# Optimization experiments

Hardware: AMD Instinct MI355X
Metric: run time of the kernel (lower is better)

## Reference

```python
import jax, jax.numpy as jnp
import numpy as np

B, N_LINKS, N_JOINTS, C_L, C_J = 4096, 33, 32, 64, 128

def setup_inputs() -> dict:
    key = jax.random.key(0)
    k1, k2, k3, k4 = jax.random.split(key, 4)
    link_feats = jax.random.normal(k1, (B, N_LINKS, C_L, 16), dtype=jnp.float32)
    joint_feats = jax.random.normal(k2, (B, N_JOINTS, C_J), dtype=jnp.float32)
    # Stacked per-joint Linear weights: [J, C_L*16, C_J], bias [J, C_J]
    fan_in = C_L * 16
    W = jax.random.normal(k3, (N_JOINTS, fan_in, C_J), dtype=jnp.float32) / np.sqrt(fan_in).astype(np.float32)
    b = jax.random.normal(k4, (N_JOINTS, C_J), dtype=jnp.float32) * 0.01
    child_idx = jnp.arange(1, N_JOINTS + 1, dtype=jnp.int64)  # child link of joint j is link j+1
    return {"link_feats": link_feats, "joint_feats": joint_feats, "W": W, "b": b, "child_idx": child_idx}

def reference(link_feats, joint_feats, W, b, child_idx):
    # Gather child-link features per joint: [B, J, C_L, 16] -> flatten to [B, J, C_L*16]
    Bsz = link_feats.shape[0]
    J = child_idx.shape[0]
    x = link_feats[:, child_idx].reshape(Bsz, J, -1)
    # Grouped GEMM over joints (replaces Python loop of tiny Linears), + bias + residual
    return jnp.einsum('bji,jio->bjo', x, W) + b[None, :, :] + joint_feats
```

## Files before the change

### kernel.cpp

```cpp
#include <hip/hip_runtime.h>

typedef __attribute__((ext_vector_type(8))) short bf16x8;
typedef __attribute__((ext_vector_type(4))) float f32x4;

#define NB    4096
#define NLINK 33
#define NJ    32
#define KTOT  1024
#define CJ    128
#define NSTEP 32

__device__ short g_Wf[NJ * KTOT * CJ];

static __device__ __forceinline__ short f2bf(float f) {
    unsigned u = __builtin_bit_cast(unsigned, f);
    unsigned r = u + 0x7FFFu + ((u >> 16) & 1u);
    return (short)(r >> 16);
}

__global__ __launch_bounds__(256) void conv_w(const float* __restrict__ W) {
    const int gid = blockIdx.x * 256 + threadIdx.x;
    const int q  = gid & 3;
    const int c  = (gid >> 2) & 127;
    const int kt = (gid >> 9) & 31;
    const int j  = gid >> 14;
    const float* src = W + ((size_t)j * KTOT + kt * 32 + q * 8) * CJ + c;
    bf16x8 v;
    #pragma unroll
    for (int e = 0; e < 8; ++e) v[e] = f2bf(src[(size_t)e * CJ]);
    reinterpret_cast<bf16x8*>(g_Wf)[gid] = v;
}

__global__ __launch_bounds__(256, 2) void joint_gemm(
    const float* __restrict__ link,
    const float* __restrict__ jf,
    const float* __restrict__ bias,
    const int*   __restrict__ child,
    float* __restrict__ out)
{
    const int tid  = threadIdx.x;
    const int lane = tid & 63;
    const int wave = tid >> 6;
    const int q    = lane >> 4;
    const int r    = lane & 15;

    const int bx = blockIdx.x;
    const int j  = bx & 31;
    const int mt = bx >> 5;
    const int row0 = mt * 128 + wave * 32;
    const int cidx = child[j];

    const float* a0 = link + ((size_t)(row0 + r) * NLINK + cidx) * KTOT + q * 8;
    const float* a1 = a0 + (size_t)16 * NLINK * KTOT;

    const bf16x8* wb = reinterpret_cast<const bf16x8*>(g_Wf);
    const size_t bb = ((size_t)j * 32 * 128 + r) * 4 + q;

    f32x4 acc[2][8] = {};

    float4 A0[4], A1[4];
    bf16x8 B0[8], B1[8];

    auto loadA = [&](float4* A, int t) {
        const float4* p0 = reinterpret_cast<const float4*>(a0 + t * 32);
        const float4* p1 = reinterpret_cast<const float4*>(a1 + t * 32);
        A[0] = p0[0]; A[1] = p0[1]; A[2] = p1[0]; A[3] = p1[1];
    };
    auto loadB = [&](bf16x8* Bv, int t) {
        const bf16x8* p = wb + bb + (size_t)t * 512;
        #pragma unroll
        for (int ni = 0; ni < 8; ++ni) Bv[ni] = p[ni * 64];
    };

    loadA(A0, 0); loadB(B0, 0);
    loadA(A1, 1); loadB(B1, 1);

    for (int t = 0; t < NSTEP; t += 2) {
        {
            bf16x8 af0, af1;
            const float* f = reinterpret_cast<const float*>(A0);
            #pragma unroll
            for (int e = 0; e < 8; ++e) { af0[e] = f2bf(f[e]); af1[e] = f2bf(f[8 + e]); }
            if (t + 2 < NSTEP) loadA(A0, t + 2);
            #pragma unroll
            for (int ni = 0; ni < 8; ++ni) {
                acc[0][ni] = __builtin_amdgcn_mfma_f32_16x16x32_bf16(af0, B0[ni], acc[0][ni], 0, 0, 0);
                acc[1][ni] = __builtin_amdgcn_mfma_f32_16x16x32_bf16(af1, B0[ni], acc[1][ni], 0, 0, 0);
            }
            if (t + 2 < NSTEP) loadB(B0, t + 2);
        }
        {
            bf16x8 af0, af1;
            const float* f = reinterpret_cast<const float*>(A1);
            #pragma unroll
            for (int e = 0; e < 8; ++e) { af0[e] = f2bf(f[e]); af1[e] = f2bf(f[8 + e]); }
            if (t + 3 < NSTEP) loadA(A1, t + 3);
            #pragma unroll
            for (int ni = 0; ni < 8; ++ni) {
                acc[0][ni] = __builtin_amdgcn_mfma_f32_16x16x32_bf16(af0, B1[ni], acc[0][ni], 0, 0, 0);
                acc[1][ni] = __builtin_amdgcn_mfma_f32_16x16x32_bf16(af1, B1[ni], acc[1][ni], 0, 0, 0);
            }
            if (t + 3 < NSTEP) loadB(B1, t + 3);
        }
    }

    float bv[8];
    #pragma unroll
    for (int ni = 0; ni < 8; ++ni) bv[ni] = bias[j * CJ + ni * 16 + r];

    #pragma unroll
    for (int mi = 0; mi < 2; ++mi) {
        #pragma unroll
        for (int rr = 0; rr < 4; ++rr) {
            const int bg = row0 + mi * 16 + q * 4 + rr;
            const size_t ob = ((size_t)bg * NJ + j) * CJ;
            #pragma unroll
            for (int ni = 0; ni < 8; ++ni) {
                const int o = ni * 16 + r;
                out[ob + o] = acc[mi][ni][rr] + bv[ni] + jf[ob + o];
            }
        }
    }
}

extern "C" void kernel_launch(void* const* d_in, const int* in_sizes, int n_in,
                              void* d_out, int out_size, void* d_ws, size_t ws_size,
                              hipStream_t stream) {
    (void)in_sizes; (void)n_in; (void)out_size; (void)d_ws; (void)ws_size;
    const float* link  = (const float*)d_in[0];
    const float* jfeat = (const float*)d_in[1];
    const float* W     = (const float*)d_in[2];
    const float* bias  = (const float*)d_in[3];
    const int*   child = (const int*)d_in[4];
    float* out = (float*)d_out;

    conv_w<<<dim3((NJ * KTOT * CJ / 8) / 256), dim3(256), 0, stream>>>(W);
    joint_gemm<<<dim3(NJ * (NB / 128)), dim3(256), 0, stream>>>(link, jfeat, bias, child, out);
}
```

Measured before the change: 191.7 us.

## Halve per-wave row tile and deepen A-row prefetch in joint GEMM

Each wave now computes a 16-row tile instead of 32, doubling the grid, and A rows are prefetched in 128-element chunks double-buffered two groups ahead. B fragments are loaded right before use instead of being software-pipelined. The intent is more memory-level parallelism on the dominant activation stream and more waves to hide latency. The cost is half the B reuse per load, so more L2 traffic for weights, and B load latency is exposed.

```diff
diff --git a/kernel.cpp b/kernel.cpp
--- a/kernel.cpp
+++ b/kernel.cpp
@@ -8,7 +8,6 @@
 #define NJ    32
 #define KTOT  1024
 #define CJ    128
-#define NSTEP 32
 
 __device__ short g_Wf[NJ * KTOT * CJ];
 
@@ -39,68 +38,59 @@
     float* __restrict__ out)
 {
     const int tid  = threadIdx.x;
-    const int lane = tid & 63;
     const int wave = tid >> 6;
-    const int q    = lane >> 4;
-    const int r    = lane & 15;
+    const int q    = (tid >> 4) & 3;
+    const int r    = tid & 15;
 
     const int bx = blockIdx.x;
     const int j  = bx & 31;
     const int mt = bx >> 5;
-    const int row0 = mt * 128 + wave * 32;
     const int cidx = child[j];
 
-    const float* a0 = link + ((size_t)(row0 + r) * NLINK + cidx) * KTOT + q * 8;
-    const float* a1 = a0 + (size_t)16 * NLINK * KTOT;
+    const int arow_idx = mt * 64 + wave * 16 + r;
+    const float* arow = link + ((size_t)arow_idx * NLINK + cidx) * KTOT + q * 8;
 
     const bf16x8* wb = reinterpret_cast<const bf16x8*>(g_Wf);
-    const size_t bb = ((size_t)j * 32 * 128 + r) * 4 + q;
+    const size_t bb = (size_t)j * 16384 + r * 4 + q;
 
-    f32x4 acc[2][8] = {};
+    f32x4  acc[8] = {};
+    float4 Ab[2][8];
 
-    float4 A0[4], A1[4];
-    bf16x8 B0[8], B1[8];
+    #pragma unroll
+    for (int i = 0; i < 4; ++i) {
+        const float4* p = reinterpret_cast<const float4*>(arow + i * 32);
+        Ab[0][i * 2] = p[0]; Ab[0][i * 2 + 1] = p[1];
+    }
+    #pragma unroll
+    for (int i = 0; i < 4; ++i) {
+        const float4* p = reinterpret_cast<const float4*>(arow + 128 + i * 32);
+        Ab[1][i * 2] = p[0]; Ab[1][i * 2 + 1] = p[1];
+    }
 
-    auto loadA = [&](float4* A, int t) {
-        const float4* p0 = reinterpret_cast<const float4*>(a0 + t * 32);
-        const float4* p1 = reinterpret_cast<const float4*>(a1 + t * 32);
-        A[0] = p0[0]; A[1] = p0[1]; A[2] = p1[0]; A[3] = p1[1];
-    };
-    auto loadB = [&](bf16x8* Bv, int t) {
-        const bf16x8* p = wb + bb + (size_t)t * 512;
+    #pragma unroll
+    for (int g = 0; g < 8; ++g) {
         #pragma unroll
-        for (int ni = 0; ni < 8; ++ni) Bv[ni] = p[ni * 64];
-    };
-
-    loadA(A0, 0); loadB(B0, 0);
-    loadA(A1, 1); loadB(B1, 1);
-
-    for (int t = 0; t < NSTEP; t += 2) {
-        {
-            bf16x8 af0, af1;
-            const float* f = reinterpret_cast<const float*>(A0);
+        for (int i = 0; i < 4; ++i) {
+            const int t = g * 4 + i;
+            bf16x8 Breg[8];
             #pragma unroll
-            for (int e = 0; e < 8; ++e) { af0[e] = f2bf(f[e]); af1[e] = f2bf(f[8 + e]); }
-            if (t + 2 < NSTEP) loadA(A0, t + 2);
+            for (int ni = 0; ni < 8; ++ni)
+                Breg[ni] = wb[bb + (size_t)t * 512 + ni * 64];
+            const float4 a0 = Ab[g & 1][i * 2];
+            const float4 a1 = Ab[g & 1][i * 2 + 1];
+            bf16x8 af;
+            af[0] = f2bf(a0.x); af[1] = f2bf(a0.y); af[2] = f2bf(a0.z); af[3] = f2bf(a0.w);
+            af[4] = f2bf(a1.x); af[5] = f2bf(a1.y); af[6] = f2bf(a1.z); af[7] = f2bf(a1.w);
             #pragma unroll
-            for (int ni = 0; ni < 8; ++ni) {
-                acc[0][ni] = __builtin_amdgcn_mfma_f32_16x16x32_bf16(af0, B0[ni], acc[0][ni], 0, 0, 0);
-                acc[1][ni] = __builtin_amdgcn_mfma_f32_16x16x32_bf16(af1, B0[ni], acc[1][ni], 0, 0, 0);
+            for (int ni = 0; ni < 8; ++ni)
+                acc[ni] = __builtin_amdgcn_mfma_f32_16x16x32_bf16(af, Breg[ni], acc[ni], 0, 0, 0);
+        }
+        if (g + 2 < 8) {
+            #pragma unroll
+            for (int i = 0; i < 4; ++i) {
+                const float4* p = reinterpret_cast<const float4*>(arow + (g + 2) * 128 + i * 32);
+                Ab[g & 1][i * 2] = p[0]; Ab[g & 1][i * 2 + 1] = p[1];
             }
-            if (t + 2 < NSTEP) loadB(B0, t + 2);
-        }
-        {
-            bf16x8 af0, af1;
-            const float* f = reinterpret_cast<const float*>(A1);
-            #pragma unroll
-            for (int e = 0; e < 8; ++e) { af0[e] = f2bf(f[e]); af1[e] = f2bf(f[8 + e]); }
-            if (t + 3 < NSTEP) loadA(A1, t + 3);
-            #pragma unroll
-            for (int ni = 0; ni < 8; ++ni) {
-                acc[0][ni] = __builtin_amdgcn_mfma_f32_16x16x32_bf16(af0, B1[ni], acc[0][ni], 0, 0, 0);
-                acc[1][ni] = __builtin_amdgcn_mfma_f32_16x16x32_bf16(af1, B1[ni], acc[1][ni], 0, 0, 0);
-            }
-            if (t + 3 < NSTEP) loadB(B1, t + 3);
         }
     }
 
@@ -109,16 +99,13 @@
     for (int ni = 0; ni < 8; ++ni) bv[ni] = bias[j * CJ + ni * 16 + r];
 
     #pragma unroll
-    for (int mi = 0; mi < 2; ++mi) {
+    for (int rr = 0; rr < 4; ++rr) {
+        const int brow = mt * 64 + wave * 16 + q * 4 + rr;
+        const size_t ob = ((size_t)brow * NJ + j) * CJ;
         #pragma unroll
-        for (int rr = 0; rr < 4; ++rr) {
-            const int bg = row0 + mi * 16 + q * 4 + rr;
-            const size_t ob = ((size_t)bg * NJ + j) * CJ;
-            #pragma unroll
-            for (int ni = 0; ni < 8; ++ni) {
-                const int o = ni * 16 + r;
-                out[ob + o] = acc[mi][ni][rr] + bv[ni] + jf[ob + o];
-            }
+        for (int ni = 0; ni < 8; ++ni) {
+            const int o = ni * 16 + r;
+            out[ob + o] = acc[ni][rr] + bv[ni] + jf[ob + o];
         }
     }
 }
@@ -135,5 +122,5 @@
     float* out = (float*)d_out;
 
     conv_w<<<dim3((NJ * KTOT * CJ / 8) / 256), dim3(256), 0, stream>>>(W);
-    joint_gemm<<<dim3(NJ * (NB / 128)), dim3(256), 0, stream>>>(link, jfeat, bias, child, out);
+    joint_gemm<<<dim3(NJ * (NB / 64)), dim3(256), 0, stream>>>(link, jfeat, bias, child, out);
 }
```

New measurement: 229.9 us. 1.2x slower.

## Stage bf16 A tile in LDS and split output columns across waves

Applied to the files above, without the earlier changes.

The block tile shrinks to 32 rows. Each block now loads its 32x256 fp32 A slice cooperatively with coalesced float4 loads, converts it to bf16 once into shared memory, and every wave reads it back through LDS. Each wave computes a 32-column slice of the output instead of all 128 columns, which cuts accumulator registers and allows 3 blocks per CU. The cost is two barriers per macro step, 4x more blocks, and W being reread from global by 4x more blocks, which adds L2 traffic.

```diff
diff --git a/kernel.cpp b/kernel.cpp
--- a/kernel.cpp
+++ b/kernel.cpp
@@ -1,6 +1,7 @@
 #include <hip/hip_runtime.h>
 
 typedef __attribute__((ext_vector_type(8))) short bf16x8;
+typedef __attribute__((ext_vector_type(4))) short bf16x4;
 typedef __attribute__((ext_vector_type(4))) float f32x4;
 
 #define NB    4096
@@ -8,7 +9,9 @@
 #define NJ    32
 #define KTOT  1024
 #define CJ    128
-#define NSTEP 32
+#define BM    32
+#define BKF   256
+#define NMAC  (KTOT / BKF)
 
 __device__ short g_Wf[NJ * KTOT * CJ];
 
@@ -31,13 +34,15 @@
     reinterpret_cast<bf16x8*>(g_Wf)[gid] = v;
 }
 
-__global__ __launch_bounds__(256, 2) void joint_gemm(
+__global__ __launch_bounds__(256, 3) void joint_gemm(
     const float* __restrict__ link,
     const float* __restrict__ jf,
     const float* __restrict__ bias,
     const int*   __restrict__ child,
     float* __restrict__ out)
 {
+    __shared__ short lA[BM * BKF];
+
     const int tid  = threadIdx.x;
     const int lane = tid & 63;
     const int wave = tid >> 6;
@@ -47,75 +52,71 @@
     const int bx = blockIdx.x;
     const int j  = bx & 31;
     const int mt = bx >> 5;
-    const int row0 = mt * 128 + wave * 32;
+    const int row0 = mt * BM;
     const int cidx = child[j];
 
-    const float* a0 = link + ((size_t)(row0 + r) * NLINK + cidx) * KTOT + q * 8;
-    const float* a1 = a0 + (size_t)16 * NLINK * KTOT;
+    const int srow = tid >> 3;
+    const int li   = tid & 7;
+    const float* abase = link + ((size_t)(row0 + srow) * NLINK + cidx) * KTOT + 4 * li;
+    short* lw0 = lA + (((li >> 1) * 32 + srow) * 8 + (li & 1) * 4);
 
     const bf16x8* wb = reinterpret_cast<const bf16x8*>(g_Wf);
-    const size_t bb = ((size_t)j * 32 * 128 + r) * 4 + q;
+    const size_t bb = ((size_t)j * 32 * 128 + wave * 32 + r) * 4 + q;
 
-    f32x4 acc[2][8] = {};
+    f32x4  acc[2][2] = {};
+    float4 Ar[8];
 
-    float4 A0[4], A1[4];
-    bf16x8 B0[8], B1[8];
-
-    auto loadA = [&](float4* A, int t) {
-        const float4* p0 = reinterpret_cast<const float4*>(a0 + t * 32);
-        const float4* p1 = reinterpret_cast<const float4*>(a1 + t * 32);
-        A[0] = p0[0]; A[1] = p0[1]; A[2] = p1[0]; A[3] = p1[1];
-    };
-    auto loadB = [&](bf16x8* Bv, int t) {
-        const bf16x8* p = wb + bb + (size_t)t * 512;
+    auto loadA = [&](int m) {
         #pragma unroll
-        for (int ni = 0; ni < 8; ++ni) Bv[ni] = p[ni * 64];
+        for (int i = 0; i < 8; ++i)
+            Ar[i] = *reinterpret_cast<const float4*>(abase + m * BKF + 32 * i);
     };
 
-    loadA(A0, 0); loadB(B0, 0);
-    loadA(A1, 1); loadB(B1, 1);
+    loadA(0);
 
-    for (int t = 0; t < NSTEP; t += 2) {
-        {
-            bf16x8 af0, af1;
-            const float* f = reinterpret_cast<const float*>(A0);
-            #pragma unroll
-            for (int e = 0; e < 8; ++e) { af0[e] = f2bf(f[e]); af1[e] = f2bf(f[8 + e]); }
-            if (t + 2 < NSTEP) loadA(A0, t + 2);
-            #pragma unroll
-            for (int ni = 0; ni < 8; ++ni) {
-                acc[0][ni] = __builtin_amdgcn_mfma_f32_16x16x32_bf16(af0, B0[ni], acc[0][ni], 0, 0, 0);
-                acc[1][ni] = __builtin_amdgcn_mfma_f32_16x16x32_bf16(af1, B0[ni], acc[1][ni], 0, 0, 0);
-            }
-            if (t + 2 < NSTEP) loadB(B0, t + 2);
+    for (int m = 0; m < NMAC; ++m) {
+        __syncthreads();
+        #pragma unroll
+        for (int i = 0; i < 8; ++i) {
+            bf16x4 v;
+            v[0] = f2bf(Ar[i].x); v[1] = f2bf(Ar[i].y);
+            v[2] = f2bf(Ar[i].z); v[3] = f2bf(Ar[i].w);
+            *reinterpret_cast<bf16x4*>(lw0 + i * 1024) = v;
         }
-        {
-            bf16x8 af0, af1;
-            const float* f = reinterpret_cast<const float*>(A1);
-            #pragma unroll
-            for (int e = 0; e < 8; ++e) { af0[e] = f2bf(f[e]); af1[e] = f2bf(f[8 + e]); }
-            if (t + 3 < NSTEP) loadA(A1, t + 3);
-            #pragma unroll
-            for (int ni = 0; ni < 8; ++ni) {
-                acc[0][ni] = __builtin_amdgcn_mfma_f32_16x16x32_bf16(af0, B1[ni], acc[0][ni], 0, 0, 0);
-                acc[1][ni] = __builtin_amdgcn_mfma_f32_16x16x32_bf16(af1, B1[ni], acc[1][ni], 0, 0, 0);
-            }
-            if (t + 3 < NSTEP) loadB(B1, t + 3);
+        __syncthreads();
+
+        bf16x8 Ball[16];
+        #pragma unroll
+        for (int ks = 0; ks < 8; ++ks) {
+            Ball[2 * ks]     = wb[bb + (size_t)(m * 8 + ks) * 512];
+            Ball[2 * ks + 1] = wb[bb + (size_t)(m * 8 + ks) * 512 + 64];
+        }
+        if (m + 1 < NMAC) loadA(m + 1);
+
+        #pragma unroll
+        for (int ks = 0; ks < 8; ++ks) {
+            const short* cb = lA + ((ks * 4 + q) * 32 + r) * 8;
+            bf16x8 a0 = *reinterpret_cast<const bf16x8*>(cb);
+            bf16x8 a1 = *reinterpret_cast<const bf16x8*>(cb + 16 * 8);
+            acc[0][0] = __builtin_amdgcn_mfma_f32_16x16x32_bf16(a0, Ball[2 * ks],     acc[0][0], 0, 0, 0);
+            acc[0][1] = __builtin_amdgcn_mfma_f32_16x16x32_bf16(a0, Ball[2 * ks + 1], acc[0][1], 0, 0, 0);
+            acc[1][0] = __builtin_amdgcn_mfma_f32_16x16x32_bf16(a1, Ball[2 * ks],     acc[1][0], 0, 0, 0);
+            acc[1][1] = __builtin_amdgcn_mfma_f32_16x16x32_bf16(a1, Ball[2 * ks + 1], acc[1][1], 0, 0, 0);
         }
     }
 
-    float bv[8];
-    #pragma unroll
-    for (int ni = 0; ni < 8; ++ni) bv[ni] = bias[j * CJ + ni * 16 + r];
+    float bv[2];
+    bv[0] = bias[j * CJ + wave * 32 + r];
+    bv[1] = bias[j * CJ + wave * 32 + 16 + r];
 
     #pragma unroll
     for (int mi = 0; mi < 2; ++mi) {
         #pragma unroll
         for (int rr = 0; rr < 4; ++rr) {
             const int bg = row0 + mi * 16 + q * 4 + rr;
-            const size_t ob = ((size_t)bg * NJ + j) * CJ;
+            const size_t ob = ((size_t)bg * NJ + j) * CJ + wave * 32;
             #pragma unroll
-            for (int ni = 0; ni < 8; ++ni) {
+            for (int ni = 0; ni < 2; ++ni) {
                 const int o = ni * 16 + r;
                 out[ob + o] = acc[mi][ni][rr] + bv[ni] + jf[ob + o];
             }
@@ -135,5 +136,5 @@
     float* out = (float*)d_out;
 
     conv_w<<<dim3((NJ * KTOT * CJ / 8) / 256), dim3(256), 0, stream>>>(W);
-    joint_gemm<<<dim3(NJ * (NB / 128)), dim3(256), 0, stream>>>(link, jfeat, bias, child, out);
+    joint_gemm<<<dim3(NJ * (NB / BM)), dim3(256), 0, stream>>>(link, jfeat, bias, child, out);
 }
```

Measured after the change: 173.6 us. -9.4%, faster.

## Split output columns across four blocks to raise occupancy in joint GEMM

Applied to the files above, without the earlier changes.

Each block now computes a 32-column slice of the 128 output channels instead of all of them, and the grid grows fourfold. The per-thread accumulator and B-register footprint shrinks, so launch bounds rise to four blocks per SIMD group, and the K loop is fully unrolled. The cost is that each A tile (link features, fp32) is loaded and converted to bf16 four times, once per column block, which multiplies global A traffic and conversion work. Some unused lambdas are left in.

```diff
diff --git a/kernel.cpp b/kernel.cpp
--- a/kernel.cpp
+++ b/kernel.cpp
@@ -8,7 +8,6 @@
 #define NJ    32
 #define KTOT  1024
 #define CJ    128
-#define NSTEP 32
 
 __device__ short g_Wf[NJ * KTOT * CJ];
 
@@ -31,7 +30,7 @@
     reinterpret_cast<bf16x8*>(g_Wf)[gid] = v;
 }
 
-__global__ __launch_bounds__(256, 2) void joint_gemm(
+__global__ __launch_bounds__(256, 4) void joint_gemm(
     const float* __restrict__ link,
     const float* __restrict__ jf,
     const float* __restrict__ bias,
@@ -46,78 +45,94 @@
 
     const int bx = blockIdx.x;
     const int j  = bx & 31;
-    const int mt = bx >> 5;
-    const int row0 = mt * 128 + wave * 32;
+    const int cb = (bx >> 5) & 3;
+    const int mt = bx >> 7;
     const int cidx = child[j];
 
+    const int row0 = mt * 128 + wave * 32;
     const float* a0 = link + ((size_t)(row0 + r) * NLINK + cidx) * KTOT + q * 8;
     const float* a1 = a0 + (size_t)16 * NLINK * KTOT;
 
     const bf16x8* wb = reinterpret_cast<const bf16x8*>(g_Wf);
-    const size_t bb = ((size_t)j * 32 * 128 + r) * 4 + q;
+    const size_t bb = (size_t)j * 16384 + ((size_t)cb * 32 + r) * 4 + q;
 
-    f32x4 acc[2][8] = {};
+    f32x4  acc[4] = {};
+    float4 A0[2], A1[2];
+    bf16x8 B0[2], B1[2];
 
-    float4 A0[4], A1[4];
-    bf16x8 B0[8], B1[8];
+    auto loadA = [&](float4* A, int ks) {
+        A[0] = *reinterpret_cast<const float4*>(a0 + ks * 32);
+        A[1] = *reinterpret_cast<const float4*>(a0 + ks * 32 + 4);
+    };
+    auto loadA2 = [&](float4* A, int ks) {
+        A[0] = *reinterpret_cast<const float4*>(a1 + ks * 32);
+        A[1] = *reinterpret_cast<const float4*>(a1 + ks * 32 + 4);
+    };
+    auto loadApair = [&](float4* A, int ks) {
+        A[0] = *reinterpret_cast<const float4*>(a0 + ks * 32);
+        A[1] = *reinterpret_cast<const float4*>(a1 + ks * 32);
+    };
+    (void)loadA; (void)loadA2; (void)loadApair;
 
-    auto loadA = [&](float4* A, int t) {
-        const float4* p0 = reinterpret_cast<const float4*>(a0 + t * 32);
-        const float4* p1 = reinterpret_cast<const float4*>(a1 + t * 32);
-        A[0] = p0[0]; A[1] = p0[1]; A[2] = p1[0]; A[3] = p1[1];
+    float4 A0a[2], A0b[2], A1a[2], A1b[2];
+    auto ldA = [&](float4* Ra, float4* Rb, int ks) {
+        Ra[0] = *reinterpret_cast<const float4*>(a0 + ks * 32);
+        Ra[1] = *reinterpret_cast<const float4*>(a0 + ks * 32 + 4);
+        Rb[0] = *reinterpret_cast<const float4*>(a1 + ks * 32);
+        Rb[1] = *reinterpret_cast<const float4*>(a1 + ks * 32 + 4);
     };
-    auto loadB = [&](bf16x8* Bv, int t) {
-        const bf16x8* p = wb + bb + (size_t)t * 512;
-        #pragma unroll
-        for (int ni = 0; ni < 8; ++ni) Bv[ni] = p[ni * 64];
+    auto ldB = [&](bf16x8* Bv, int ks) {
+        Bv[0] = wb[bb + (size_t)ks * 512];
+        Bv[1] = wb[bb + (size_t)ks * 512 + 64];
+    };
+    auto cvt = [&](const float4* Ra, const float4* Rb, bf16x8& f0, bf16x8& f1) {
+        f0[0] = f2bf(Ra[0].x); f0[1] = f2bf(Ra[0].y); f0[2] = f2bf(Ra[0].z); f0[3] = f2bf(Ra[0].w);
+        f0[4] = f2bf(Ra[1].x); f0[5] = f2bf(Ra[1].y); f0[6] = f2bf(Ra[1].z); f0[7] = f2bf(Ra[1].w);
+        f1[0] = f2bf(Rb[0].x); f1[1] = f2bf(Rb[0].y); f1[2] = f2bf(Rb[0].z); f1[3] = f2bf(Rb[0].w);
+        f1[4] = f2bf(Rb[1].x); f1[5] = f2bf(Rb[1].y); f1[6] = f2bf(Rb[1].z); f1[7] = f2bf(Rb[1].w);
     };
 
-    loadA(A0, 0); loadB(B0, 0);
-    loadA(A1, 1); loadB(B1, 1);
+    ldA(A0a, A0b, 0); ldB(B0, 0);
+    ldA(A1a, A1b, 1); ldB(B1, 1);
 
-    for (int t = 0; t < NSTEP; t += 2) {
+    #pragma unroll
+    for (int g = 0; g < 16; ++g) {
         {
             bf16x8 af0, af1;
-            const float* f = reinterpret_cast<const float*>(A0);
-            #pragma unroll
-            for (int e = 0; e < 8; ++e) { af0[e] = f2bf(f[e]); af1[e] = f2bf(f[8 + e]); }
-            if (t + 2 < NSTEP) loadA(A0, t + 2);
-            #pragma unroll
-            for (int ni = 0; ni < 8; ++ni) {
-                acc[0][ni] = __builtin_amdgcn_mfma_f32_16x16x32_bf16(af0, B0[ni], acc[0][ni], 0, 0, 0);
-                acc[1][ni] = __builtin_amdgcn_mfma_f32_16x16x32_bf16(af1, B0[ni], acc[1][ni], 0, 0, 0);
-            }
-            if (t + 2 < NSTEP) loadB(B0, t + 2);
+            cvt(A0a, A0b, af0, af1);
+            if (g < 15) ldA(A0a, A0b, 2 * g + 2);
+            acc[0] = __builtin_amdgcn_mfma_f32_16x16x32_bf16(af0, B0[0], acc[0], 0, 0, 0);
+            acc[1] = __builtin_amdgcn_mfma_f32_16x16x32_bf16(af0, B0[1], acc[1], 0, 0, 0);
+            acc[2] = __builtin_amdgcn_mfma_f32_16x16x32_bf16(af1, B0[0], acc[2], 0, 0, 0);
+            acc[3] = __builtin_amdgcn_mfma_f32_16x16x32_bf16(af1, B0[1], acc[3], 0, 0, 0);
+            if (g < 15) ldB(B0, 2 * g + 2);
         }
         {
             bf16x8 af0, af1;
-            const float* f = reinterpret_cast<const float*>(A1);
-            #pragma unroll
-            for (int e = 0; e < 8; ++e) { af0[e] = f2bf(f[e]); af1[e] = f2bf(f[8 + e]); }
-            if (t + 3 < NSTEP) loadA(A1, t + 3);
-            #pragma unroll
-            for (int ni = 0; ni < 8; ++ni) {
-                acc[0][ni] = __builtin_amdgcn_mfma_f32_16x16x32_bf16(af0, B1[ni], acc[0][ni], 0, 0, 0);
-                acc[1][ni] = __builtin_amdgcn_mfma_f32_16x16x32_bf16(af1, B1[ni], acc[1][ni], 0, 0, 0);
-            }
-            if (t + 3 < NSTEP) loadB(B1, t + 3);
+            cvt(A1a, A1b, af0, af1);
+            if (g < 15) ldA(A1a, A1b, 2 * g + 3);
+            acc[0] = __builtin_amdgcn_mfma_f32_16x16x32_bf16(af0, B1[0], acc[0], 0, 0, 0);
+            acc[1] = __builtin_amdgcn_mfma_f32_16x16x32_bf16(af0, B1[1], acc[1], 0, 0, 0);
+            acc[2] = __builtin_amdgcn_mfma_f32_16x16x32_bf16(af1, B1[0], acc[2], 0, 0, 0);
+            acc[3] = __builtin_amdgcn_mfma_f32_16x16x32_bf16(af1, B1[1], acc[3], 0, 0, 0);
+            if (g < 15) ldB(B1, 2 * g + 3);
         }
     }
 
-    float bv[8];
-    #pragma unroll
-    for (int ni = 0; ni < 8; ++ni) bv[ni] = bias[j * CJ + ni * 16 + r];
+    float bv[2];
+    bv[0] = bias[j * CJ + cb * 32 + r];
+    bv[1] = bias[j * CJ + cb * 32 + 16 + r];
 
     #pragma unroll
     for (int mi = 0; mi < 2; ++mi) {
         #pragma unroll
         for (int rr = 0; rr < 4; ++rr) {
             const int bg = row0 + mi * 16 + q * 4 + rr;
-            const size_t ob = ((size_t)bg * NJ + j) * CJ;
+            const size_t ob = ((size_t)bg * NJ + j) * CJ + cb * 32;
             #pragma unroll
-            for (int ni = 0; ni < 8; ++ni) {
+            for (int ni = 0; ni < 2; ++ni) {
                 const int o = ni * 16 + r;
-                out[ob + o] = acc[mi][ni][rr] + bv[ni] + jf[ob + o];
+                out[ob + o] = acc[mi * 2 + ni][rr] + bv[ni] + jf[ob + o];
             }
         }
     }
@@ -135,5 +150,5 @@
     float* out = (float*)d_out;
 
     conv_w<<<dim3((NJ * KTOT * CJ / 8) / 256), dim3(256), 0, stream>>>(W);
-    joint_gemm<<<dim3(NJ * (NB / 128)), dim3(256), 0, stream>>>(link, jfeat, bias, child, out);
+    joint_gemm<<<dim3(NJ * 4 * (NB / 128)), dim3(256), 0, stream>>>(link, jfeat, bias, child, out);
 }
```

New measurement: 342.6 us. 78.8% more time.
